# Performance work log

Measured on AMD Instinct MI355X. Metric: run time of the kernel, lower is better.

The kernel has to match this reference:

```python
import jax, jax.numpy as jnp
import numpy as np

B, S, D, H, F = 64, 512, 1024, 1024, 1024  # note: module requires H == D
EPS = 1e-6


def setup_inputs() -> dict:
    key = jax.random.key(0)
    ks = jax.random.split(key, 14)
    p = lambda k, shape: 0.02 * jax.random.normal(k, shape, dtype=jnp.float32)
    return {
        "hidden_state": jax.random.normal(ks[0], (B, S, D), dtype=jnp.float32),
        "field_hidden_state": jax.random.normal(ks[1], (B, S, F), dtype=jnp.float32),
        "input": jax.random.normal(ks[2], (B, D), dtype=jnp.float32),
        "finished": jnp.zeros((B, 1), dtype=bool),
        "W1": p(ks[3], (H, D)), "b1": p(ks[4], (H,)),
        "W2": p(ks[5], (H, D)), "b2": p(ks[6], (H,)),
        "W3": p(ks[7], (H, 2 * D)), "b3": p(ks[8], (H,)),
        "W4": p(ks[9], (H, F)), "b4": p(ks[10], (H,)),
        "W5": p(ks[11], (H, D)), "b5": p(ks[12], (H,)),
    }


def _norm_over_seq(w):
    # manual exp/max/sum softmax over seq dim (axis 0) with 1e-6 guard, as in torch
    w = jnp.exp(w - jnp.max(w, axis=0, keepdims=True))
    return w / (EPS + jnp.sum(w, axis=0, keepdims=True))


def reference(hidden_state, field_hidden_state, input, finished,
              W1, b1, W2, b2, W3, b3, W4, b4, W5, b5):
    hs = jnp.transpose(hidden_state, (1, 0, 2))        # [S, B, D]
    fs = jnp.transpose(field_hidden_state, (1, 0, 2))  # [S, B, F]
    phi_h = jnp.tanh(hs @ W1.T + b1)                   # [S, B, H]
    phi_f = jnp.tanh(fs @ W4.T + b4)                   # [S, B, H]

    gamma_h = jnp.tanh(input @ W2.T + b2)              # [B, H]
    weights = _norm_over_seq(jnp.sum(phi_h * gamma_h, axis=2, keepdims=True))  # [S, B, 1]

    alpha_h = jnp.tanh(input @ W5.T + b5)              # [B, H]
    field_w = _norm_over_seq(jnp.sum(phi_f * alpha_h, axis=2, keepdims=True))  # [S, B, 1]

    wf = weights * field_w
    weights = wf / (EPS + jnp.sum(wf, axis=0, keepdims=True))  # [S, B, 1]

    context = jnp.sum(hs * weights, axis=0)            # [B, D]
    out = jnp.concatenate([context, input], axis=-1) @ W3.T + b3  # [B, H]
    out = jnp.where(finished, jnp.zeros_like(out), out)
    return out, weights
```

## Files before the change

### kernel.cpp

```cpp
#include <hip/hip_runtime.h>

#define EPS 1e-6f

typedef _Float16 f16;
typedef _Float16 f16x4 __attribute__((ext_vector_type(4)));
typedef _Float16 f16x8 __attribute__((ext_vector_type(8)));
typedef float f32x4 __attribute__((ext_vector_type(4)));

#define PHASE_BAR() do { __builtin_amdgcn_sched_barrier(0); \
                         __builtin_amdgcn_s_barrier();      \
                         __builtin_amdgcn_sched_barrier(0); } while (0)

__device__ __forceinline__ float tanh_fast(float x) {
    float e = __expf(2.0f * x);
    return 1.0f - 2.0f / (e + 1.0f);
}

__global__ __launch_bounds__(256) void conv_kernel(
    const float4* __restrict__ src, f16x4* __restrict__ dst, int n4)
{
    int stride = gridDim.x * 256;
    for (int i = blockIdx.x * 256 + threadIdx.x; i < n4; i += stride) {
        float4 v = src[i];
        f16x4 o; o[0]=(f16)v.x; o[1]=(f16)v.y; o[2]=(f16)v.z; o[3]=(f16)v.w;
        dst[i] = o;
    }
}

__global__ __launch_bounds__(256) void gamal_kernel(
    const float* __restrict__ inp,
    const float* __restrict__ W2, const float* __restrict__ b2,
    const float* __restrict__ W5, const float* __restrict__ b5,
    float* __restrict__ gamm, float* __restrict__ alph)
{
    const float* W  = blockIdx.y ? W5 : W2;
    const float* bs = blockIdx.y ? b5 : b2;
    float* dst      = blockIdx.y ? alph : gamm;
    int wid = threadIdx.x >> 6, lane = threadIdx.x & 63;
    int p = blockIdx.x * 4 + wid;
    int b = p >> 10, h = p & 1023;
    const float4* wr = (const float4*)(W + (size_t)h * 1024);
    const float4* xr = (const float4*)(inp + (size_t)b * 1024);
    float acc = 0.f;
    #pragma unroll
    for (int j = 0; j < 4; ++j) {
        float4 w4 = wr[lane + 64 * j];
        float4 x4 = xr[lane + 64 * j];
        acc += w4.x * x4.x + w4.y * x4.y + w4.z * x4.z + w4.w * x4.w;
    }
    #pragma unroll
    for (int o = 32; o; o >>= 1) acc += __shfl_xor(acc, o);
    if (lane == 0) dst[p] = tanh_fast(acc + bs[h]);
}

__global__ __launch_bounds__(512, 1) void gemm_logits_kernel(
    const f16* __restrict__ Ah,
    const f16* __restrict__ Wh,
    const float* __restrict__ b1, const float* __restrict__ b4,
    const float* __restrict__ gamm, const float* __restrict__ alph,
    float* __restrict__ Lpart)
{
    __shared__ __align__(16) char smA[2][32768];
    __shared__ __align__(16) char smW[2][32768];
    __shared__ float rowpart[256][4];

    const int lin = blockIdx.x;
    const int swz = (lin & 7) * 128 + (lin >> 3);
    const int mat = swz >> 9;
    const int rem = swz & 511;
    const int m_blk = rem >> 2;
    const int nc = rem & 3;
    const int m0 = m_blk << 8;
    const int hc0 = nc << 8;
    const int bidx = m_blk >> 1;

    const f16* A = Ah + (size_t)mat * 33554432;
    const f16* W = Wh + (size_t)mat * 1048576;
    const float* bv = mat ? b4 : b1;
    const float* gv = mat ? alph : gamm;

    const int t = threadIdx.x;
    const int lane = t & 63;
    const int wv = t >> 6;
    const int wr = wv >> 2;
    const int wc = wv & 3;
    const int c16 = lane & 15;
    const int kg = lane >> 4;

    const int lrow = lane >> 3, lslot = lane & 7;
    const int kchunk = lslot ^ lrow;

    const int swzr = (c16 & 7) << 4;
    const int aoffb = (wr * 128 + c16) * 128;
    const int woffb = (wc * 64 + c16) * 128;
    const int kg16 = kg * 16;

    f32x4 acc[8][4];
    #pragma unroll
    for (int i = 0; i < 8; ++i)
        #pragma unroll
        for (int j = 0; j < 4; ++j) acc[i][j] = (f32x4){0.f, 0.f, 0.f, 0.f};

    auto stageA = [&](int kt, char* buf, int h) {
        #pragma unroll
        for (int j = 0; j < 2; ++j) {
            int q = wv * 2 + j;
            int r = (q >> 3) * 128 + h * 64 + (q & 7) * 8;
            const f16* src = A + (size_t)(m0 + r + lrow) * 1024 + kt * 64 + kchunk * 8;
            __builtin_amdgcn_global_load_lds(
                (const __attribute__((address_space(1))) void*)src,
                (__attribute__((address_space(3))) void*)(buf + r * 128), 16, 0, 0);
        }
    };
    auto stageW = [&](int kt, char* buf, int h) {
        #pragma unroll
        for (int j = 0; j < 2; ++j) {
            int q = wv * 2 + j;
            int r = (q >> 2) * 64 + h * 32 + (q & 3) * 8;
            const f16* src = W + (size_t)(hc0 + r + lrow) * 1024 + kt * 64 + kchunk * 8;
            __builtin_amdgcn_global_load_lds(
                (const __attribute__((address_space(1))) void*)src,
                (__attribute__((address_space(3))) void*)(buf + r * 128), 16, 0, 0);
        }
    };

    stageA(0, smA[0], 0); stageA(0, smA[0], 1);
    stageW(0, smW[0], 0); stageW(0, smW[0], 1);
    stageA(1, smA[1], 0);
    __builtin_amdgcn_sched_barrier(0);
    asm volatile("s_waitcnt vmcnt(2)" ::: "memory");
    PHASE_BAR();

    for (int kt = 0; kt < 16; ++kt) {
        char* aC = smA[kt & 1];
        char* wC = smW[kt & 1];
        char* aN = smA[(kt & 1) ^ 1];
        char* wN = smW[(kt & 1) ^ 1];
        const int kt1 = kt < 15 ? kt + 1 : 15;
        const int kt2 = kt < 14 ? kt + 2 : 15;

        f16x8 af[8], bf0[4], bf1[4];

        stageA(kt1, aN, 1);
        #pragma unroll
        for (int mi = 0; mi < 4; ++mi)
            #pragma unroll
            for (int kk = 0; kk < 2; ++kk)
                af[mi * 2 + kk] = *(const f16x8*)(aC + aoffb + mi * 2048 + ((kk * 64 + kg16) ^ swzr));
        #pragma unroll
        for (int ni = 0; ni < 2; ++ni)
            #pragma unroll
            for (int kk = 0; kk < 2; ++kk)
                bf0[ni * 2 + kk] = *(const f16x8*)(wC + woffb + ni * 2048 + ((kk * 64 + kg16) ^ swzr));
        __builtin_amdgcn_s_setprio(1);
        #pragma unroll
        for (int ni = 0; ni < 2; ++ni)
            #pragma unroll
            for (int mi = 0; mi < 4; ++mi)
                #pragma unroll
                for (int kk = 0; kk < 2; ++kk)
                    acc[mi][ni] = __builtin_amdgcn_mfma_f32_16x16x32_f16(af[mi * 2 + kk], bf0[ni * 2 + kk], acc[mi][ni], 0, 0, 0);
        __builtin_amdgcn_s_setprio(0);
        PHASE_BAR();

        stageW(kt1, wN, 0);
        #pragma unroll
        for (int ni = 0; ni < 2; ++ni)
            #pragma unroll
            for (int kk = 0; kk < 2; ++kk)
                bf1[ni * 2 + kk] = *(const f16x8*)(wC + woffb + 4096 + ni * 2048 + ((kk * 64 + kg16) ^ swzr));
        __builtin_amdgcn_s_setprio(1);
        #pragma unroll
        for (int ni = 0; ni < 2; ++ni)
            #pragma unroll
            for (int mi = 0; mi < 4; ++mi)
                #pragma unroll
                for (int kk = 0; kk < 2; ++kk)
                    acc[mi][ni + 2] = __builtin_amdgcn_mfma_f32_16x16x32_f16(af[mi * 2 + kk], bf1[ni * 2 + kk], acc[mi][ni + 2], 0, 0, 0);
        __builtin_amdgcn_s_setprio(0);
        PHASE_BAR();

        stageW(kt1, wN, 1);
        #pragma unroll
        for (int mi = 0; mi < 4; ++mi)
            #pragma unroll
            for (int kk = 0; kk < 2; ++kk)
                af[mi * 2 + kk] = *(const f16x8*)(aC + aoffb + 8192 + mi * 2048 + ((kk * 64 + kg16) ^ swzr));
        __builtin_amdgcn_s_setprio(1);
        #pragma unroll
        for (int ni = 0; ni < 2; ++ni)
            #pragma unroll
            for (int mi = 0; mi < 4; ++mi)
                #pragma unroll
                for (int kk = 0; kk < 2; ++kk)
                    acc[mi + 4][ni] = __builtin_amdgcn_mfma_f32_16x16x32_f16(af[mi * 2 + kk], bf0[ni * 2 + kk], acc[mi + 4][ni], 0, 0, 0);
        __builtin_amdgcn_s_setprio(0);
        PHASE_BAR();

        stageA(kt2, aC, 0);
        __builtin_amdgcn_sched_barrier(0);
        __builtin_amdgcn_s_setprio(1);
        #pragma unroll
        for (int ni = 0; ni < 2; ++ni)
            #pragma unroll
            for (int mi = 0; mi < 4; ++mi)
                #pragma unroll
                for (int kk = 0; kk < 2; ++kk)
                    acc[mi + 4][ni + 2] = __builtin_amdgcn_mfma_f32_16x16x32_f16(af[mi * 2 + kk], bf1[ni * 2 + kk], acc[mi + 4][ni + 2], 0, 0, 0);
        __builtin_amdgcn_s_setprio(0);
        __builtin_amdgcn_sched_barrier(0);
        asm volatile("s_waitcnt vmcnt(2)" ::: "memory");
        PHASE_BAR();
    }

    float g[4], bb[4];
    #pragma unroll
    for (int ni = 0; ni < 4; ++ni) {
        int h = hc0 + wc * 64 + ni * 16 + c16;
        g[ni]  = gv[(bidx << 10) + h];
        bb[ni] = bv[h];
    }
    #pragma unroll
    for (int mi = 0; mi < 8; ++mi) {
        #pragma unroll
        for (int q = 0; q < 4; ++q) {
            float v = tanh_fast(acc[mi][0][q] + bb[0]) * g[0]
                    + tanh_fast(acc[mi][1][q] + bb[1]) * g[1]
                    + tanh_fast(acc[mi][2][q] + bb[2]) * g[2]
                    + tanh_fast(acc[mi][3][q] + bb[3]) * g[3];
            v += __shfl_xor(v, 1);
            v += __shfl_xor(v, 2);
            v += __shfl_xor(v, 4);
            v += __shfl_xor(v, 8);
            if (c16 == 0)
                rowpart[wr * 128 + mi * 16 + kg * 4 + q][wc] = v;
        }
    }
    __syncthreads();
    if (t < 256)
        Lpart[(size_t)(mat * 4 + nc) * 32768 + m0 + t] =
            rowpart[t][0] + rowpart[t][1] + rowpart[t][2] + rowpart[t][3];
}

__device__ __forceinline__ float blockMax(float v, float* sm) {
    #pragma unroll
    for (int o = 32; o; o >>= 1) v = fmaxf(v, __shfl_xor(v, o));
    if ((threadIdx.x & 63) == 0) sm[threadIdx.x >> 6] = v;
    __syncthreads();
    v = fmaxf(fmaxf(sm[0], sm[1]), fmaxf(sm[2], sm[3]));
    __syncthreads();
    return v;
}
__device__ __forceinline__ float blockSum(float v, float* sm) {
    #pragma unroll
    for (int o = 32; o; o >>= 1) v += __shfl_xor(v, o);
    if ((threadIdx.x & 63) == 0) sm[threadIdx.x >> 6] = v;
    __syncthreads();
    v = sm[0] + sm[1] + sm[2] + sm[3];
    __syncthreads();
    return v;
}

__global__ __launch_bounds__(256) void softmax_combine_kernel(
    const float* __restrict__ Lp,
    float* __restrict__ wfin, float* __restrict__ dout)
{
    __shared__ float sm[4];
    int b = blockIdx.x, t = threadIdx.x;
    float h0 = 0.f, h1 = 0.f, f0 = 0.f, f1 = 0.f;
    #pragma unroll
    for (int nc = 0; nc < 4; ++nc) {
        h0 += Lp[nc * 32768 + b * 512 + t];
        h1 += Lp[nc * 32768 + b * 512 + 256 + t];
        f0 += Lp[(4 + nc) * 32768 + b * 512 + t];
        f1 += Lp[(4 + nc) * 32768 + b * 512 + 256 + t];
    }
    float mh = blockMax(fmaxf(h0, h1), sm);
    float mf = blockMax(fmaxf(f0, f1), sm);
    float e0 = __expf(h0 - mh), e1 = __expf(h1 - mh);
    float q0 = __expf(f0 - mf), q1 = __expf(f1 - mf);
    float sh = blockSum(e0 + e1, sm);
    float sf = blockSum(q0 + q1, sm);
    float wh0 = e0 / (EPS + sh), wh1 = e1 / (EPS + sh);
    float wq0 = q0 / (EPS + sf), wq1 = q1 / (EPS + sf);
    float c0 = wh0 * wq0, c1 = wh1 * wq1;
    float sc = blockSum(c0 + c1, sm);
    float r0 = c0 / (EPS + sc), r1 = c1 / (EPS + sc);
    wfin[b * 512 + t]       = r0;
    wfin[b * 512 + 256 + t] = r1;
    dout[65536 + t * 64 + b]         = r0;
    dout[65536 + (256 + t) * 64 + b] = r1;
}

__global__ __launch_bounds__(256) void context_kernel(
    const f16* __restrict__ Ah, const float* __restrict__ wgt,
    float* __restrict__ ctxpart)
{
    int dq = blockIdx.x;
    int b  = blockIdx.y;
    int sh = blockIdx.z;
    int t = threadIdx.x;
    int ss = t >> 6, ds = t & 63;
    __shared__ float part[4][64][8];
    float a[8] = {0,0,0,0,0,0,0,0};
    int sBase = sh * 256 + ss * 64;
    const f16* hp = Ah + (size_t)b * 524288 + dq * 512 + ds * 8;
    for (int i = 0; i < 64; ++i) {
        int s = sBase + i;
        float w = wgt[b * 512 + s];
        f16x8 v = *(const f16x8*)(hp + (size_t)s * 1024);
        #pragma unroll
        for (int j = 0; j < 8; ++j) a[j] += w * (float)v[j];
    }
    #pragma unroll
    for (int j = 0; j < 8; ++j) part[ss][ds][j] = a[j];
    __syncthreads();
    if (ss == 0) {
        #pragma unroll
        for (int j = 0; j < 8; ++j) {
            float o = part[0][ds][j] + part[1][ds][j] + part[2][ds][j] + part[3][ds][j];
            ctxpart[(size_t)sh * 65536 + b * 1024 + dq * 512 + ds * 8 + j] = o;
        }
    }
}

__global__ __launch_bounds__(256) void out_kernel(
    const float* __restrict__ ctxpart, const float* __restrict__ inp,
    const float* __restrict__ W3, const float* __restrict__ b3,
    const unsigned char* __restrict__ fin, float* __restrict__ out)
{
    int t = threadIdx.x, wid = t >> 6, lane = t & 63;
    int h = blockIdx.x * 4 + wid;
    __shared__ __align__(16) float xs[2048];
    float4* xsv = (float4*)xs;
    float4 wreg[8];
    const float4* w3r = (const float4*)(W3 + (size_t)h * 2048);
    #pragma unroll
    for (int j = 0; j < 8; ++j) wreg[j] = w3r[lane + 64 * j];
    const float4* cp = (const float4*)ctxpart;
    const float4* xp = (const float4*)inp;
    for (int b = 0; b < 64; ++b) {
        __syncthreads();
        {
            float4 c0 = cp[b * 256 + t];
            float4 c1 = cp[16384 + b * 256 + t];
            float4 cc; cc.x = c0.x + c1.x; cc.y = c0.y + c1.y;
            cc.z = c0.z + c1.z; cc.w = c0.w + c1.w;
            xsv[t] = cc;
            xsv[256 + t] = xp[b * 256 + t];
        }
        __syncthreads();
        float acc = 0.f;
        #pragma unroll
        for (int j = 0; j < 8; ++j) {
            float4 x = xsv[lane + 64 * j];
            acc += wreg[j].x * x.x + wreg[j].y * x.y + wreg[j].z * x.z + wreg[j].w * x.w;
        }
        #pragma unroll
        for (int o = 32; o; o >>= 1) acc += __shfl_xor(acc, o);
        if (lane == 0) out[b * 1024 + h] = fin[b] ? 0.f : (acc + b3[h]);
    }
}

extern "C" void kernel_launch(void* const* d_in, const int* in_sizes, int n_in,
                              void* d_out, int out_size, void* d_ws, size_t ws_size,
                              hipStream_t stream)
{
    const float* hidden = (const float*)d_in[0];
    const float* field  = (const float*)d_in[1];
    const float* input  = (const float*)d_in[2];
    const unsigned char* fin = (const unsigned char*)d_in[3];
    const float* W1 = (const float*)d_in[4];
    const float* b1 = (const float*)d_in[5];
    const float* W2 = (const float*)d_in[6];
    const float* b2 = (const float*)d_in[7];
    const float* W3 = (const float*)d_in[8];
    const float* b3 = (const float*)d_in[9];
    const float* W4 = (const float*)d_in[10];
    const float* b4 = (const float*)d_in[11];
    const float* W5 = (const float*)d_in[12];
    const float* b5 = (const float*)d_in[13];
    float* out = (float*)d_out;

    char* ws = (char*)d_ws;
    float* Lpart = (float*)(ws);
    float* wfin  = (float*)(ws + 2097152);
    float* gamm  = (float*)(ws + 2228224);
    float* alph  = (float*)(ws + 2490368);
    float* ctxp  = (float*)(ws + 2752512);
    f16*   Wh    = (f16*)(ws + 3276800);
    f16*   Ah    = (f16*)(ws + 7471104);

    conv_kernel<<<4096, 256, 0, stream>>>((const float4*)hidden, (f16x4*)Ah, 8388608);
    conv_kernel<<<4096, 256, 0, stream>>>((const float4*)field,  (f16x4*)(Ah + 33554432), 8388608);
    conv_kernel<<<1024, 256, 0, stream>>>((const float4*)W1, (f16x4*)Wh, 262144);
    conv_kernel<<<1024, 256, 0, stream>>>((const float4*)W4, (f16x4*)(Wh + 1048576), 262144);

    gamal_kernel<<<dim3(16384, 2), 256, 0, stream>>>(input, W2, b2, W5, b5, gamm, alph);
    gemm_logits_kernel<<<1024, 512, 0, stream>>>(Ah, Wh, b1, b4, gamm, alph, Lpart);
    softmax_combine_kernel<<<64, 256, 0, stream>>>(Lpart, wfin, out);
    context_kernel<<<dim3(2, 64, 2), 256, 0, stream>>>(Ah, wfin, ctxp);
    out_kernel<<<256, 256, 0, stream>>>(ctxp, input, W3, b3, fin, out);
}
```

Measured before the change: 365.3 us.

## Merge conversion launches, reuse weight rows in gamma kernel, reschedule GEMM pipeline

Folds the four fp32-to-fp16 conversion launches into one grid-stride kernel. The gamma/alpha GEMV now keeps each weight row in registers and reuses it across 8 batch rows, cutting redundant weight reads. The logits GEMM main loop is reorganised: it prefetches only one k-tile ahead, issues each LDS read before its global-to-LDS stage, and splits every phase barrier into separate barrier and waitcnt steps. The new barrier/waitcnt placement may either hide load latency better or add stalls.

```diff
diff --git a/kernel.cpp b/kernel.cpp
--- a/kernel.cpp
+++ b/kernel.cpp
@@ -1,29 +1,34 @@
 #include <hip/hip_runtime.h>
 
 #define EPS 1e-6f
+#define SB() __builtin_amdgcn_sched_barrier(0)
 
 typedef _Float16 f16;
 typedef _Float16 f16x4 __attribute__((ext_vector_type(4)));
 typedef _Float16 f16x8 __attribute__((ext_vector_type(8)));
 typedef float f32x4 __attribute__((ext_vector_type(4)));
 
-#define PHASE_BAR() do { __builtin_amdgcn_sched_barrier(0); \
-                         __builtin_amdgcn_s_barrier();      \
-                         __builtin_amdgcn_sched_barrier(0); } while (0)
-
 __device__ __forceinline__ float tanh_fast(float x) {
     float e = __expf(2.0f * x);
     return 1.0f - 2.0f / (e + 1.0f);
 }
 
-__global__ __launch_bounds__(256) void conv_kernel(
-    const float4* __restrict__ src, f16x4* __restrict__ dst, int n4)
-{
-    int stride = gridDim.x * 256;
-    for (int i = blockIdx.x * 256 + threadIdx.x; i < n4; i += stride) {
-        float4 v = src[i];
+__global__ __launch_bounds__(256) void convall_kernel(
+    const float4* __restrict__ hidden, const float4* __restrict__ field,
+    const float4* __restrict__ W1, const float4* __restrict__ W4,
+    f16x4* __restrict__ Ah, f16x4* __restrict__ Af,
+    f16x4* __restrict__ Wh1, f16x4* __restrict__ Wh4)
+{
+    const int stride = gridDim.x * 256;
+    for (int i = blockIdx.x * 256 + threadIdx.x; i < 17301504; i += stride) {
+        const float4* s; f16x4* d; int off;
+        if (i < 8388608)       { s = hidden; d = Ah;  off = i; }
+        else if (i < 16777216) { s = field;  d = Af;  off = i - 8388608; }
+        else if (i < 17039360) { s = W1;     d = Wh1; off = i - 16777216; }
+        else                   { s = W4;     d = Wh4; off = i - 17039360; }
+        float4 v = s[off];
         f16x4 o; o[0]=(f16)v.x; o[1]=(f16)v.y; o[2]=(f16)v.z; o[3]=(f16)v.w;
-        dst[i] = o;
+        d[off] = o;
     }
 }
 
@@ -37,24 +42,31 @@
     const float* bs = blockIdx.y ? b5 : b2;
     float* dst      = blockIdx.y ? alph : gamm;
     int wid = threadIdx.x >> 6, lane = threadIdx.x & 63;
-    int p = blockIdx.x * 4 + wid;
-    int b = p >> 10, h = p & 1023;
+    int hb = blockIdx.x >> 3;
+    int bb = blockIdx.x & 7;
+    int h = hb * 4 + wid;
+    int b0 = bb * 8;
     const float4* wr = (const float4*)(W + (size_t)h * 1024);
-    const float4* xr = (const float4*)(inp + (size_t)b * 1024);
-    float acc = 0.f;
-    #pragma unroll
-    for (int j = 0; j < 4; ++j) {
-        float4 w4 = wr[lane + 64 * j];
-        float4 x4 = xr[lane + 64 * j];
-        acc += w4.x * x4.x + w4.y * x4.y + w4.z * x4.z + w4.w * x4.w;
-    }
-    #pragma unroll
-    for (int o = 32; o; o >>= 1) acc += __shfl_xor(acc, o);
-    if (lane == 0) dst[p] = tanh_fast(acc + bs[h]);
+    float4 wreg[4];
+    #pragma unroll
+    for (int j = 0; j < 4; ++j) wreg[j] = wr[lane + 64 * j];
+    float bias = bs[h];
+    for (int b = b0; b < b0 + 8; ++b) {
+        const float4* xr = (const float4*)(inp + (size_t)b * 1024);
+        float acc = 0.f;
+        #pragma unroll
+        for (int j = 0; j < 4; ++j) {
+            float4 x4 = xr[lane + 64 * j];
+            acc += wreg[j].x * x4.x + wreg[j].y * x4.y + wreg[j].z * x4.z + wreg[j].w * x4.w;
+        }
+        #pragma unroll
+        for (int o = 32; o; o >>= 1) acc += __shfl_xor(acc, o);
+        if (lane == 0) dst[b * 1024 + h] = tanh_fast(acc + bias);
+    }
 }
 
 __global__ __launch_bounds__(512, 1) void gemm_logits_kernel(
-    const f16* __restrict__ Ah,
+    const f16* __restrict__ Ahh,
     const f16* __restrict__ Wh,
     const float* __restrict__ b1, const float* __restrict__ b4,
     const float* __restrict__ gamm, const float* __restrict__ alph,
@@ -74,7 +86,7 @@
     const int hc0 = nc << 8;
     const int bidx = m_blk >> 1;
 
-    const f16* A = Ah + (size_t)mat * 33554432;
+    const f16* A = Ahh + (size_t)mat * 33554432;
     const f16* W = Wh + (size_t)mat * 1048576;
     const float* bv = mat ? b4 : b1;
     const float* gv = mat ? alph : gamm;
@@ -124,24 +136,24 @@
         }
     };
 
-    stageA(0, smA[0], 0); stageA(0, smA[0], 1);
-    stageW(0, smW[0], 0); stageW(0, smW[0], 1);
-    stageA(1, smA[1], 0);
-    __builtin_amdgcn_sched_barrier(0);
-    asm volatile("s_waitcnt vmcnt(2)" ::: "memory");
-    PHASE_BAR();
+    stageA(0, smA[0], 0);
+    stageW(0, smW[0], 0);
+    stageW(0, smW[0], 1);
+    stageA(0, smA[0], 1);
+    SB();
+    asm volatile("s_waitcnt vmcnt(4)" ::: "memory");
+    SB();
+    __builtin_amdgcn_s_barrier();
 
     for (int kt = 0; kt < 16; ++kt) {
         char* aC = smA[kt & 1];
         char* wC = smW[kt & 1];
-        char* aN = smA[(kt & 1) ^ 1];
-        char* wN = smW[(kt & 1) ^ 1];
+        char* aN = smA[(kt + 1) & 1];
+        char* wN = smW[(kt + 1) & 1];
         const int kt1 = kt < 15 ? kt + 1 : 15;
-        const int kt2 = kt < 14 ? kt + 2 : 15;
-
-        f16x8 af[8], bf0[4], bf1[4];
-
-        stageA(kt1, aN, 1);
+
+        f16x8 af[8], wf0[4], wf1[4];
+
         #pragma unroll
         for (int mi = 0; mi < 4; ++mi)
             #pragma unroll
@@ -151,7 +163,12 @@
         for (int ni = 0; ni < 2; ++ni)
             #pragma unroll
             for (int kk = 0; kk < 2; ++kk)
-                bf0[ni * 2 + kk] = *(const f16x8*)(wC + woffb + ni * 2048 + ((kk * 64 + kg16) ^ swzr));
+                wf0[ni * 2 + kk] = *(const f16x8*)(wC + woffb + ni * 2048 + ((kk * 64 + kg16) ^ swzr));
+        stageA(kt1, aN, 0);
+        SB();
+        __builtin_amdgcn_s_barrier();
+        asm volatile("s_waitcnt lgkmcnt(0)" ::: "memory");
+        SB();
         __builtin_amdgcn_s_setprio(1);
         #pragma unroll
         for (int ni = 0; ni < 2; ++ni)
@@ -159,16 +176,23 @@
             for (int mi = 0; mi < 4; ++mi)
                 #pragma unroll
                 for (int kk = 0; kk < 2; ++kk)
-                    acc[mi][ni] = __builtin_amdgcn_mfma_f32_16x16x32_f16(af[mi * 2 + kk], bf0[ni * 2 + kk], acc[mi][ni], 0, 0, 0);
+                    acc[mi][ni] = __builtin_amdgcn_mfma_f32_16x16x32_f16(af[mi * 2 + kk], wf0[ni * 2 + kk], acc[mi][ni], 0, 0, 0);
         __builtin_amdgcn_s_setprio(0);
-        PHASE_BAR();
-
+        SB();
+        asm volatile("s_waitcnt vmcnt(4)" ::: "memory");
+        SB();
+        __builtin_amdgcn_s_barrier();
+
+        #pragma unroll
+        for (int ni = 0; ni < 2; ++ni)
+            #pragma unroll
+            for (int kk = 0; kk < 2; ++kk)
+                wf1[ni * 2 + kk] = *(const f16x8*)(wC + woffb + 4096 + ni * 2048 + ((kk * 64 + kg16) ^ swzr));
         stageW(kt1, wN, 0);
-        #pragma unroll
-        for (int ni = 0; ni < 2; ++ni)
-            #pragma unroll
-            for (int kk = 0; kk < 2; ++kk)
-                bf1[ni * 2 + kk] = *(const f16x8*)(wC + woffb + 4096 + ni * 2048 + ((kk * 64 + kg16) ^ swzr));
+        SB();
+        __builtin_amdgcn_s_barrier();
+        asm volatile("s_waitcnt lgkmcnt(0)" ::: "memory");
+        SB();
         __builtin_amdgcn_s_setprio(1);
         #pragma unroll
         for (int ni = 0; ni < 2; ++ni)
@@ -176,16 +200,23 @@
             for (int mi = 0; mi < 4; ++mi)
                 #pragma unroll
                 for (int kk = 0; kk < 2; ++kk)
-                    acc[mi][ni + 2] = __builtin_amdgcn_mfma_f32_16x16x32_f16(af[mi * 2 + kk], bf1[ni * 2 + kk], acc[mi][ni + 2], 0, 0, 0);
+                    acc[mi][ni + 2] = __builtin_amdgcn_mfma_f32_16x16x32_f16(af[mi * 2 + kk], wf1[ni * 2 + kk], acc[mi][ni + 2], 0, 0, 0);
         __builtin_amdgcn_s_setprio(0);
-        PHASE_BAR();
-
-        stageW(kt1, wN, 1);
+        SB();
+        asm volatile("s_waitcnt vmcnt(4)" ::: "memory");
+        SB();
+        __builtin_amdgcn_s_barrier();
+
         #pragma unroll
         for (int mi = 0; mi < 4; ++mi)
             #pragma unroll
             for (int kk = 0; kk < 2; ++kk)
                 af[mi * 2 + kk] = *(const f16x8*)(aC + aoffb + 8192 + mi * 2048 + ((kk * 64 + kg16) ^ swzr));
+        stageW(kt1, wN, 1);
+        SB();
+        __builtin_amdgcn_s_barrier();
+        asm volatile("s_waitcnt lgkmcnt(0)" ::: "memory");
+        SB();
         __builtin_amdgcn_s_setprio(1);
         #pragma unroll
         for (int ni = 0; ni < 2; ++ni)
@@ -193,12 +224,15 @@
             for (int mi = 0; mi < 4; ++mi)
                 #pragma unroll
                 for (int kk = 0; kk < 2; ++kk)
-                    acc[mi + 4][ni] = __builtin_amdgcn_mfma_f32_16x16x32_f16(af[mi * 2 + kk], bf0[ni * 2 + kk], acc[mi + 4][ni], 0, 0, 0);
+                    acc[mi + 4][ni] = __builtin_amdgcn_mfma_f32_16x16x32_f16(af[mi * 2 + kk], wf0[ni * 2 + kk], acc[mi + 4][ni], 0, 0, 0);
         __builtin_amdgcn_s_setprio(0);
-        PHASE_BAR();
-
-        stageA(kt2, aC, 0);
-        __builtin_amdgcn_sched_barrier(0);
+        SB();
+        __builtin_amdgcn_s_barrier();
+
+        stageA(kt1, aN, 1);
+        SB();
+        __builtin_amdgcn_s_barrier();
+        SB();
         __builtin_amdgcn_s_setprio(1);
         #pragma unroll
         for (int ni = 0; ni < 2; ++ni)
@@ -206,11 +240,12 @@
             for (int mi = 0; mi < 4; ++mi)
                 #pragma unroll
                 for (int kk = 0; kk < 2; ++kk)
-                    acc[mi + 4][ni + 2] = __builtin_amdgcn_mfma_f32_16x16x32_f16(af[mi * 2 + kk], bf1[ni * 2 + kk], acc[mi + 4][ni + 2], 0, 0, 0);
+                    acc[mi + 4][ni + 2] = __builtin_amdgcn_mfma_f32_16x16x32_f16(af[mi * 2 + kk], wf1[ni * 2 + kk], acc[mi + 4][ni + 2], 0, 0, 0);
         __builtin_amdgcn_s_setprio(0);
-        __builtin_amdgcn_sched_barrier(0);
-        asm volatile("s_waitcnt vmcnt(2)" ::: "memory");
-        PHASE_BAR();
+        SB();
+        asm volatile("s_waitcnt vmcnt(4)" ::: "memory");
+        SB();
+        __builtin_amdgcn_s_barrier();
     }
 
     float g[4], bb[4];
@@ -391,12 +426,13 @@
     f16*   Wh    = (f16*)(ws + 3276800);
     f16*   Ah    = (f16*)(ws + 7471104);
 
-    conv_kernel<<<4096, 256, 0, stream>>>((const float4*)hidden, (f16x4*)Ah, 8388608);
-    conv_kernel<<<4096, 256, 0, stream>>>((const float4*)field,  (f16x4*)(Ah + 33554432), 8388608);
-    conv_kernel<<<1024, 256, 0, stream>>>((const float4*)W1, (f16x4*)Wh, 262144);
-    conv_kernel<<<1024, 256, 0, stream>>>((const float4*)W4, (f16x4*)(Wh + 1048576), 262144);
-
-    gamal_kernel<<<dim3(16384, 2), 256, 0, stream>>>(input, W2, b2, W5, b5, gamm, alph);
+    convall_kernel<<<8192, 256, 0, stream>>>(
+        (const float4*)hidden, (const float4*)field,
+        (const float4*)W1, (const float4*)W4,
+        (f16x4*)Ah, (f16x4*)(Ah + 33554432),
+        (f16x4*)Wh, (f16x4*)(Wh + 1048576));
+
+    gamal_kernel<<<dim3(2048, 2), 256, 0, stream>>>(input, W2, b2, W5, b5, gamm, alph);
     gemm_logits_kernel<<<1024, 512, 0, stream>>>(Ah, Wh, b1, b4, gamm, alph, Lpart);
     softmax_combine_kernel<<<64, 256, 0, stream>>>(Lpart, wfin, out);
     context_kernel<<<dim3(2, 64, 2), 256, 0, stream>>>(Ah, wfin, ctxp);
```

New measurement: 332.9 us. -8.9%, faster.
